# Optimization experiments

Measured on AMD Instinct MI355X. Metric: run time of the kernel, lower is better.

Reference implementation:

```python
import jax, jax.numpy as jnp
import numpy as np

B, N1, N2, C, P, H, MLP = 8, 4096, 4096, 512, 256, 8, 2048
HD = C // H  # head dim = 64
EPS = 1e-12


def _l2norm(x):
    # torch F.normalize(dim=-1): x / max(||x||_2, eps)
    n = jnp.sqrt(jnp.sum(x * x, axis=-1, keepdims=True))
    return x / jnp.maximum(n, EPS)


def setup_inputs() -> dict:
    key = jax.random.key(0)
    ks = jax.random.split(key, 8)
    w = lambda i, shape: jax.random.normal(ks[i], shape, jnp.float32) * 0.02
    return {
        "x1": jax.random.normal(ks[0], (B, N1, C), jnp.float32),
        "x2": jax.random.normal(ks[1], (B, N2, C), jnp.float32),
        "Wq": w(2, (C, C)), "bq": jnp.zeros((C,), jnp.float32),
        "Wkv": w(3, (C, 2 * C)), "bkv": jnp.zeros((2 * C,), jnp.float32),
        # proj_k and proj_v share ONE Linear(N_2, proj_size) in the source
        "Wp": w(4, (N2, P)), "bp": jnp.zeros((P,), jnp.float32),
        "pos_q": jnp.zeros((1, N1, C), jnp.float32),
        "pos_k": jnp.zeros((1, N2, C), jnp.float32),
        "temperature": jnp.ones((H, 1, 1), jnp.float32),
        "W1": w(5, (C, MLP)), "b1": jnp.zeros((MLP,), jnp.float32),
        "W2": w(6, (MLP, C)), "b2": jnp.zeros((C,), jnp.float32),
    }


def reference(x1, x2, Wq, bq, Wkv, bkv, Wp, bp, pos_q, pos_k, temperature,
              W1, b1, W2, b2):
    # q += pos_embed_q is in-place in torch, so q_skip includes pos embedding
    q = x1 @ Wq + bq + pos_q                      # [B,N1,C]
    q_skip = q
    kv = x2 @ Wkv + bkv                           # [B,N2,2C]
    k = kv[..., :C] + pos_k                       # [B,N2,C]
    v = kv[..., C:]                               # [B,N2,C]

    qh = q.reshape(B, N1, H, HD).transpose(0, 2, 1, 3)   # [B,H,N1,hd]
    kh = k.reshape(B, N2, H, HD).transpose(0, 2, 1, 3)   # [B,H,N2,hd]
    vh = v.reshape(B, N2, H, HD).transpose(0, 2, 1, 3)   # [B,H,N2,hd]

    # project K^T and V^T along the sequence axis (shared weights)
    kp = jnp.einsum('bhnd,np->bhdp', kh, Wp) + bp        # [B,H,hd,P]
    vp_t = jnp.einsum('bhnd,np->bhdp', vh, Wp) + bp      # [B,H,hd,P]

    attn = jnp.einsum('bhqd,bhdp->bhqp', qh, kp) * temperature  # [B,H,N1,P]
    attn = jax.nn.softmax(attn, axis=-1)                 # dropout: eval mode

    x = jnp.einsum('bhqp,bhdp->bhqd', attn, vp_t)        # [B,H,N1,hd]
    # source does permute(0,3,1,2).reshape(B,N1,C) -- replicate exactly
    x = x.transpose(0, 3, 1, 2).reshape(B, N1, C)

    x = _l2norm(x + q_skip)                              # Add & L2-Norm
    h = jax.nn.gelu(x @ W1 + b1, approximate=False)      # nn.GELU (exact)
    out = _l2norm(h @ W2 + b2 + x)                       # FFN -> Add & L2-Norm
    return out
```

## Files before the change

kernel.cpp:

```cpp
#include <hip/hip_runtime.h>
#include <hip/hip_bf16.h>
#include <math.h>

#define B_    8
#define N1_   4096
#define N2_   4096
#define C_    512
#define P_    256
#define H_    8
#define MLP_  2048
#define HD_   64

typedef __hip_bfloat16 bf16;
typedef __attribute__((ext_vector_type(8))) short short8;
typedef __attribute__((ext_vector_type(4))) float f32x4;

__device__ __forceinline__ float bf2f(bf16 v) { return __bfloat162float(v); }
__device__ __forceinline__ bf16  f2bf(float v) { return __float2bfloat16(v); }
__device__ __forceinline__ float ubf2f(unsigned short u) {
  union { float f; unsigned int i; } cv; cv.i = ((unsigned int)u) << 16; return cv.f;
}
__device__ __forceinline__ unsigned short f2bfu(float v) {
  union { bf16 b; unsigned short u; } cv; cv.b = __float2bfloat16(v); return cv.u;
}
__device__ __forceinline__ float gelu_fast(float x) {
  const float u = fabsf(x) * 0.70710678118654752f;
  const float t = __builtin_amdgcn_rcpf(__builtin_fmaf(0.3275911f, u, 1.0f));
  float p = __builtin_fmaf(1.061405429f, t, -1.453152027f);
  p = __builtin_fmaf(p, t, 1.421413741f);
  p = __builtin_fmaf(p, t, -0.284496736f);
  p = __builtin_fmaf(p, t, 0.254829592f);
  p *= t;
  const float e = __expf(-u * u);
  float erfv = __builtin_fmaf(-p, e, 1.0f);
  erfv = (x < 0.0f) ? -erfv : erfv;
  return 0.5f * x * (1.0f + erfv);
}

__device__ __forceinline__ void gload16(const void* g, void* l) {
  __builtin_amdgcn_global_load_lds(
      (const __attribute__((address_space(1))) void*)g,
      (__attribute__((address_space(3))) void*)l, 16, 0, 0);
}

__global__ __launch_bounds__(256) void f2b_kernel(
    const float* __restrict__ in, bf16* __restrict__ out, int n4)
{
  int i = blockIdx.x * 256 + threadIdx.x;
  const int stride = gridDim.x * 256;
  for (; i < n4; i += stride) {
    const float4 v = ((const float4*)in)[i];
    ushort4 o;
    o.x = f2bfu(v.x); o.y = f2bfu(v.y); o.z = f2bfu(v.z); o.w = f2bfu(v.w);
    ((ushort4*)out)[i] = o;
  }
}

__global__ __launch_bounds__(256) void transpose_f2b_kernel(
    const float* __restrict__ in, bf16* __restrict__ out, int K, int N, int ldin)
{
  __shared__ float tile[32][33];
  const int kb = blockIdx.y * 32, nb = blockIdx.x * 32;
  const int tx = threadIdx.x & 31, ty = threadIdx.x >> 5;
  #pragma unroll
  for (int i = 0; i < 4; ++i)
    tile[ty + 8 * i][tx] = in[(size_t)(kb + ty + 8 * i) * ldin + nb + tx];
  __syncthreads();
  #pragma unroll
  for (int i = 0; i < 4; ++i)
    out[(size_t)(nb + ty + 8 * i) * K + kb + tx] = f2bf(tile[tx][ty + 8 * i]);
}

template<int BN, int OUTF32, int ACT, int POS, int TRANSC>
__global__ __launch_bounds__(256) void mfma_gemm_kernel(
    const bf16* __restrict__ A, const bf16* __restrict__ Bt,
    const float* __restrict__ bias, const float* __restrict__ pos, int posmask,
    void* __restrict__ Cv, int M, int N, int K)
{
  constexpr int WGN = BN / 64;
  constexpr int WGR = 4 / WGN;
  constexpr int FM  = 128 / (16 * WGR);
  __shared__ bf16 As[128 * 32];
  __shared__ bf16 Bs[BN * 32];
  const int t  = threadIdx.x;
  const int l  = t & 63;
  const int w  = t >> 6;
  const int wr = w / WGN, wc = w % WGN;
  const int lr = l & 15, kg = l >> 4;

  const int gx  = gridDim.x;
  const int nwg = gx * gridDim.y;
  const int h   = blockIdx.y * gx + blockIdx.x;
  int bx = blockIdx.x, by = blockIdx.y;
  if ((nwg & 7) == 0) {
    const int tid = (h & 7) * (nwg >> 3) + (h >> 3);
    bx = tid % gx; by = tid / gx;
  }
  const int m0 = by * 128, n0 = bx * BN;

  const bf16* ga = A  + (size_t)(m0 + (t >> 2)) * K + (t & 3) * 8;
  const bf16* gb = Bt + (size_t)(n0 + (t >> 2)) * K + (t & 3) * 8;
  char* asl = (char*)As + t * 16;
  char* bsl = (char*)Bs + t * 16;

  f32x4 acc[FM][4] = {};

  for (int k0 = 0; k0 < K; k0 += 32) {
    gload16(ga, asl);
    gload16(ga + (size_t)64 * K, asl + 4096);
    gload16(gb, bsl);
    if (BN == 128) gload16(gb + (size_t)64 * K, bsl + 4096);
    ga += 32; gb += 32;
    __syncthreads();
    short8 af[FM], bfv[4];
    #pragma unroll
    for (int i = 0; i < FM; ++i)
      af[i] = *(const short8*)&As[(wr * (FM * 16) + i * 16 + lr) * 32 + kg * 8];
    #pragma unroll
    for (int j = 0; j < 4; ++j)
      bfv[j] = *(const short8*)&Bs[(wc * 64 + j * 16 + lr) * 32 + kg * 8];
    #pragma unroll
    for (int i = 0; i < FM; ++i)
      #pragma unroll
      for (int j = 0; j < 4; ++j)
        acc[i][j] = __builtin_amdgcn_mfma_f32_16x16x32_bf16(
            af[i], bfv[j], acc[i][j], 0, 0, 0);
    __syncthreads();
  }

  #pragma unroll
  for (int i = 0; i < FM; ++i) {
    #pragma unroll
    for (int j = 0; j < 4; ++j) {
      const int n = n0 + wc * 64 + j * 16 + lr;
      const float bv = bias[n];
      if (TRANSC) {
        const int mb = m0 + wr * (FM * 16) + i * 16 + kg * 4;
        ushort4 pk;
        #pragma unroll
        for (int r = 0; r < 4; ++r) {
          const int m = mb + r;
          float v = acc[i][j][r] + bv;
          if (POS) v += pos[(size_t)(m & posmask) * N + n];
          ((unsigned short*)&pk)[r] = f2bfu(v);
        }
        *(ushort4*)&((bf16*)Cv)[((size_t)(mb >> 12) * N + n) * (size_t)N1_ + (mb & 4095)] = pk;
      } else {
        #pragma unroll
        for (int r = 0; r < 4; ++r) {
          const int m = m0 + wr * (FM * 16) + i * 16 + kg * 4 + r;
          float v = acc[i][j][r] + bv;
          if (POS) v += pos[(size_t)(m & posmask) * N + n];
          if (ACT) v = gelu_fast(v);
          if (OUTF32) ((float*)Cv)[(size_t)m * N + n] = v;
          else        ((bf16*)Cv)[(size_t)m * N + n] = f2bf(v);
        }
      }
    }
  }
}

template<int BIASM>
__global__ __launch_bounds__(256) void proj_kernel(
    const bf16* __restrict__ A, const bf16* __restrict__ Bt,
    const float* __restrict__ bias, bf16* __restrict__ Cb,
    int M, int N, int K, long aBatch, long bBatch, long cBatch)
{
  __shared__ bf16 As[64 * 32];
  __shared__ bf16 Bs[64 * 32];
  const int t = threadIdx.x, l = t & 63, w = t >> 6;
  const int wr = w >> 1, wc = w & 1;
  const int lr = l & 15, kg = l >> 4;
  const int z = blockIdx.z;
  const int m0 = blockIdx.y * 64, n0 = blockIdx.x * 64;
  const bf16* ga = A  + (size_t)z * aBatch + (size_t)(m0 + (t >> 2)) * K + (t & 3) * 8;
  const bf16* gb = Bt + (size_t)z * bBatch + (size_t)(n0 + (t >> 2)) * K + (t & 3) * 8;
  char* asl = (char*)As + t * 16;
  char* bsl = (char*)Bs + t * 16;
  f32x4 acc[2][2] = {};
  for (int k0 = 0; k0 < K; k0 += 32) {
    gload16(ga, asl);
    gload16(gb, bsl);
    ga += 32; gb += 32;
    __syncthreads();
    short8 af[2], bfr[2];
    #pragma unroll
    for (int i = 0; i < 2; ++i)
      af[i] = *(const short8*)&As[(wr * 32 + i * 16 + lr) * 32 + kg * 8];
    #pragma unroll
    for (int j = 0; j < 2; ++j)
      bfr[j] = *(const short8*)&Bs[(wc * 32 + j * 16 + lr) * 32 + kg * 8];
    #pragma unroll
    for (int i = 0; i < 2; ++i)
      #pragma unroll
      for (int j = 0; j < 2; ++j)
        acc[i][j] = __builtin_amdgcn_mfma_f32_16x16x32_bf16(
            af[i], bfr[j], acc[i][j], 0, 0, 0);
    __syncthreads();
  }
  #pragma unroll
  for (int i = 0; i < 2; ++i)
    #pragma unroll
    for (int j = 0; j < 2; ++j) {
      const int n = n0 + wc * 32 + j * 16 + lr;
      #pragma unroll
      for (int r = 0; r < 4; ++r) {
        const int m = m0 + wr * 32 + i * 16 + kg * 4 + r;
        const float v = acc[i][j][r] + (BIASM ? bias[m] : bias[n]);
        Cb[(size_t)z * cBatch + (size_t)m * N + n] = f2bf(v);
      }
    }
}

__global__ __launch_bounds__(256) void attn_mfma_kernel(
    const bf16* __restrict__ qb, const bf16* __restrict__ kpT,
    const bf16* __restrict__ vp, const float* __restrict__ temp,
    bf16* __restrict__ xatT)
{
  __shared__ bf16 qs[64 * 64];
  __shared__ bf16 us[256 * 64];
  __shared__ bf16 vs[64 * 256];
  const int t = threadIdx.x, w = t >> 6, l = t & 63;
  const int lr = l & 15, kg = l >> 4;
  const int b = blockIdx.z, h = blockIdx.y;
  const int q0 = blockIdx.x * 64;
  const int bh = b * H_ + h;
  const float tv = temp[h];

  {
    const int rowb = t >> 3, ch = t & 7;
    #pragma unroll
    for (int p = 0; p < 2; ++p) {
      const int r = rowb + 32 * p;
      const short8 v = *(const short8*)(qb + ((size_t)(b * N1_ + q0 + r)) * C_ + h * HD_ + ch * 8);
      *(short8*)((char*)qs + ((r * 128 + ch * 16) ^ ((r & 7) << 4))) = v;
    }
    const bf16* kpb = kpT + (size_t)bh * (P_ * HD_);
    #pragma unroll
    for (int p = 0; p < 8; ++p) {
      const int r = rowb + 32 * p;
      const short8 v = *(const short8*)(kpb + r * HD_ + ch * 8);
      *(short8*)((char*)us + ((r * 128 + ch * 16) ^ ((r & 7) << 4))) = v;
    }
    const bf16* vpb = vp + (size_t)bh * (HD_ * P_);
    const int rowv = t >> 5, chv = t & 31;
    #pragma unroll
    for (int p = 0; p < 8; ++p) {
      const int r = rowv + 8 * p;
      const short8 v = *(const short8*)(vpb + r * P_ + chv * 8);
      *(short8*)((char*)vs + ((r * 512 + chv * 16) ^ ((r & 7) << 4))) = v;
    }
  }
  __syncthreads();

  short8 aq[2];
  {
    const int row = w * 16 + lr;
    const int sw = (row & 7) << 4;
    aq[0] = *(const short8*)((const char*)qs + ((row * 128 +  0 + kg * 16) ^ sw));
    aq[1] = *(const short8*)((const char*)qs + ((row * 128 + 64 + kg * 16) ^ sw));
  }
  f32x4 s[16] = {};
  #pragma unroll
  for (int j = 0; j < 16; ++j) {
    const int row = j * 16 + lr;
    const int sw = (row & 7) << 4;
    const short8 b0 = *(const short8*)((const char*)us + ((row * 128 +  0 + kg * 16) ^ sw));
    const short8 b1 = *(const short8*)((const char*)us + ((row * 128 + 64 + kg * 16) ^ sw));
    s[j] = __builtin_amdgcn_mfma_f32_16x16x32_bf16(aq[0], b0, s[j], 0, 0, 0);
    s[j] = __builtin_amdgcn_mfma_f32_16x16x32_bf16(aq[1], b1, s[j], 0, 0, 0);
  }

  float inv_[4];
  #pragma unroll
  for (int j = 0; j < 16; ++j)
    #pragma unroll
    for (int r = 0; r < 4; ++r) s[j][r] *= tv;
  #pragma unroll
  for (int r = 0; r < 4; ++r) {
    float m = s[0][r];
    #pragma unroll
    for (int j = 1; j < 16; ++j) m = fmaxf(m, s[j][r]);
    #pragma unroll
    for (int off = 1; off < 16; off <<= 1) m = fmaxf(m, __shfl_xor(m, off));
    float sum = 0.f;
    #pragma unroll
    for (int j = 0; j < 16; ++j) { s[j][r] = __expf(s[j][r] - m); sum += s[j][r]; }
    #pragma unroll
    for (int off = 1; off < 16; off <<= 1) sum += __shfl_xor(sum, off);
    inv_[r] = 1.0f / sum;
  }
  __syncthreads();

  #pragma unroll
  for (int r = 0; r < 4; ++r) {
    const int q = w * 16 + kg * 4 + r;
    const int sw = (q & 7) << 4;
    #pragma unroll
    for (int j = 0; j < 16; ++j) {
      const int p = j * 16 + lr;
      ((unsigned short*)us)[((q * 512 + p * 2) ^ sw) >> 1] = f2bfu(s[j][r] * inv_[r]);
    }
  }
  __syncthreads();

  f32x4 o[4] = {};
  #pragma unroll
  for (int kc = 0; kc < 8; ++kc) {
    const int qrow = w * 16 + lr;
    const short8 pb = *(const short8*)((const char*)us +
        ((qrow * 512 + kc * 64 + kg * 16) ^ ((qrow & 7) << 4)));
    #pragma unroll
    for (int i = 0; i < 4; ++i) {
      const int drow = i * 16 + lr;
      const short8 vb = *(const short8*)((const char*)vs +
          ((drow * 512 + kc * 64 + kg * 16) ^ ((drow & 7) << 4)));
      o[i] = __builtin_amdgcn_mfma_f32_16x16x32_bf16(vb, pb, o[i], 0, 0, 0);
    }
  }
  const int qq = q0 + w * 16 + lr;
  bf16* ob = xatT + (size_t)bh * (HD_ * (size_t)N1_) + qq;
  #pragma unroll
  for (int i = 0; i < 4; ++i)
    #pragma unroll
    for (int r = 0; r < 4; ++r) {
      const int d = i * 16 + kg * 4 + r;
      ob[(size_t)d * N1_] = f2bf(o[i][r]);
    }
}

__global__ __launch_bounds__(256) void norm1_kernel(
    const bf16* __restrict__ xatT, const bf16* __restrict__ qb,
    bf16* __restrict__ xb)
{
  const int row = blockIdx.x;
  const int b = row >> 12, np = row & 4095;
  const int d = np >> 6, h = (np >> 3) & 7, qhi = np & 7;
  const int c = threadIdx.x * 2;
  const size_t tbase = ((size_t)(b * H_ + h) * HD_ + d) * N1_ + qhi * 512 + c;
  const size_t qbase = (size_t)row * C_ + c;
  const ushort2 xa = *(const ushort2*)((const unsigned short*)xatT + tbase);
  const ushort2 qa = *(const ushort2*)((const unsigned short*)qb + qbase);
  float v0 = ubf2f(xa.x) + ubf2f(qa.x);
  float v1 = ubf2f(xa.y) + ubf2f(qa.y);
  float ss = v0 * v0 + v1 * v1;
  #pragma unroll
  for (int off = 32; off > 0; off >>= 1) ss += __shfl_xor(ss, off);
  __shared__ float sw[4];
  if ((threadIdx.x & 63) == 0) sw[threadIdx.x >> 6] = ss;
  __syncthreads();
  const float tot = sw[0] + sw[1] + sw[2] + sw[3];
  const float scale = 1.0f / fmaxf(sqrtf(tot), 1e-12f);
  ushort2 o;
  o.x = f2bfu(v0 * scale);
  o.y = f2bfu(v1 * scale);
  *(ushort2*)((unsigned short*)xb + qbase) = o;
}

__global__ __launch_bounds__(256) void norm2_kernel(
    const float* __restrict__ yb, const bf16* __restrict__ xb,
    float* __restrict__ outp)
{
  const int row = blockIdx.x;
  const int c0 = threadIdx.x, c1 = threadIdx.x + 256;
  float v0 = yb[(size_t)row * C_ + c0] + bf2f(xb[(size_t)row * C_ + c0]);
  float v1 = yb[(size_t)row * C_ + c1] + bf2f(xb[(size_t)row * C_ + c1]);
  float ss = v0 * v0 + v1 * v1;
  #pragma unroll
  for (int off = 32; off > 0; off >>= 1) ss += __shfl_xor(ss, off);
  __shared__ float sw[4];
  if ((threadIdx.x & 63) == 0) sw[threadIdx.x >> 6] = ss;
  __syncthreads();
  const float tot = sw[0] + sw[1] + sw[2] + sw[3];
  const float scale = 1.0f / fmaxf(sqrtf(tot), 1e-12f);
  outp[(size_t)row * C_ + c0] = v0 * scale;
  outp[(size_t)row * C_ + c1] = v1 * scale;
}

extern "C" void kernel_launch(void* const* d_in, const int* in_sizes, int n_in,
                              void* d_out, int out_size, void* d_ws, size_t ws_size,
                              hipStream_t stream)
{
  const float* x1   = (const float*)d_in[0];
  const float* x2   = (const float*)d_in[1];
  const float* Wq   = (const float*)d_in[2];
  const float* bq   = (const float*)d_in[3];
  const float* Wkv  = (const float*)d_in[4];
  const float* bkv  = (const float*)d_in[5];
  const float* Wp   = (const float*)d_in[6];
  const float* bp   = (const float*)d_in[7];
  const float* posq = (const float*)d_in[8];
  const float* posk = (const float*)d_in[9];
  const float* temp = (const float*)d_in[10];
  const float* W1   = (const float*)d_in[11];
  const float* b1   = (const float*)d_in[12];
  const float* W2   = (const float*)d_in[13];
  const float* b2   = (const float*)d_in[14];

  char* ws = (char*)d_ws;
  bf16*  Abuf = (bf16*)(ws);
  bf16*  Bbuf = (bf16*)(ws + 33554432);
  bf16*  Cbuf = (bf16*)(ws + 67108864);
  bf16*  kpT  = (bf16*)(ws + 100663296);
  bf16*  vpb  = (bf16*)(ws + 102760448);
  bf16*  WpT  = (bf16*)(ws + 104857600);
  bf16*  Wqt  = (bf16*)(ws + 106954752);
  bf16*  Wkt  = (bf16*)(ws + 107479040);
  bf16*  Wvt  = (bf16*)(ws + 108003328);
  float* outp = (float*)d_out;

  int CH;
  size_t w1t_off, w2t_off, yb_off;
  if (ws_size >= 239075328UL) {
    CH = 32768; w1t_off = 167772160UL; w2t_off = 169869312UL; yb_off = 171966464UL;
  } else if (ws_size >= 138412032UL) {
    CH = 16384; w1t_off = 100663296UL; w2t_off = 102760448UL; yb_off = 104857600UL;
  } else {
    CH = 8192;  w1t_off = 100663296UL; w2t_off = 102760448UL; yb_off = 106954752UL;
  }
  bf16*  W1t = (bf16*)(ws + w1t_off);
  bf16*  W2t = (bf16*)(ws + w2t_off);
  float* yb  = (float*)(ws + yb_off);

  const dim3 blk(256);
  const int Mrows = B_ * N1_;
  bf16* xatT = Bbuf;
  bf16* xb   = Abuf;
  bf16* hb   = Bbuf;
  bf16* qb   = Cbuf;

  f2b_kernel<<<dim3(2048), blk, 0, stream>>>(x2, Abuf, (B_ * N2_ * C_) / 4);
  transpose_f2b_kernel<<<dim3(16, 16), blk, 0, stream>>>(Wkv,      Wkt, C_, C_, 2 * C_);
  transpose_f2b_kernel<<<dim3(16, 16), blk, 0, stream>>>(Wkv + C_, Wvt, C_, C_, 2 * C_);
  transpose_f2b_kernel<<<dim3(16, 16), blk, 0, stream>>>(Wq,       Wqt, C_, C_, C_);
  transpose_f2b_kernel<<<dim3(8, 128), blk, 0, stream>>>(Wp,       WpT, N2_, P_, P_);

  mfma_gemm_kernel<128,0,0,1,1><<<dim3(C_/128, Mrows/128), blk, 0, stream>>>(
      Abuf, Wkt, bkv, posk, N2_ - 1, Cbuf, Mrows, C_, C_);
  proj_kernel<1><<<dim3(1, 4, B_*H_), blk, 0, stream>>>(
      WpT, Cbuf, bp, kpT, P_, HD_, N2_, 0L, (long)HD_*N2_, (long)P_*HD_);
  mfma_gemm_kernel<128,0,0,0,1><<<dim3(C_/128, Mrows/128), blk, 0, stream>>>(
      Abuf, Wvt, bkv + C_, nullptr, 0, Cbuf, Mrows, C_, C_);
  proj_kernel<0><<<dim3(4, 1, B_*H_), blk, 0, stream>>>(
      Cbuf, WpT, bp, vpb, HD_, P_, N2_, (long)HD_*N2_, 0L, (long)HD_*P_);
  f2b_kernel<<<dim3(2048), blk, 0, stream>>>(x1, Abuf, (B_ * N1_ * C_) / 4);
  mfma_gemm_kernel<128,0,0,1,0><<<dim3(C_/128, Mrows/128), blk, 0, stream>>>(
      Abuf, Wqt, bq, posq, N1_ - 1, qb, Mrows, C_, C_);
  attn_mfma_kernel<<<dim3(N1_/64, H_, B_), blk, 0, stream>>>(
      qb, kpT, vpb, temp, xatT);
  transpose_f2b_kernel<<<dim3(64, 16), blk, 0, stream>>>(W1, W1t, C_,   MLP_, MLP_);
  transpose_f2b_kernel<<<dim3(16, 64), blk, 0, stream>>>(W2, W2t, MLP_, C_,   C_);
  norm1_kernel<<<dim3(Mrows), blk, 0, stream>>>(xatT, qb, xb);
  for (int c = 0; c < Mrows / CH; ++c) {
    const bf16* xc = xb + (size_t)c * CH * C_;
    mfma_gemm_kernel<128,0,1,0,0><<<dim3(MLP_/128, CH/128), blk, 0, stream>>>(
        xc, W1t, b1, nullptr, 0, hb, CH, MLP_, C_);
    mfma_gemm_kernel<128,1,0,0,0><<<dim3(C_/128, CH/128), blk, 0, stream>>>(
        hb, W2t, b2, nullptr, 0, yb, CH, C_, MLP_);
    norm2_kernel<<<dim3(CH), blk, 0, stream>>>(
        yb, xc, outp + (size_t)c * CH * C_);
  }
}
```

Baseline: 773.4 us.

## Double-buffer LDS in GEMM and projection kernels; fuse K/V GEMMs

Both the main MFMA GEMM and the projection kernel now use two LDS buffers. The next K-slice is loaded while the current one is computed, hiding global-load latency behind the MFMAs. The separate K and V input GEMMs are merged into one GEMM over the concatenated Wkv, with the transposed output split into two buffers (K into Cbuf, V into Bbuf). This removes one kernel launch and one re-read of x2, at the cost of doubled LDS per block, which may lower occupancy.

```diff
diff --git a/kernel.cpp b/kernel.cpp
--- a/kernel.cpp
+++ b/kernel.cpp
@@ -75,13 +75,13 @@
 __global__ __launch_bounds__(256) void mfma_gemm_kernel(
     const bf16* __restrict__ A, const bf16* __restrict__ Bt,
     const float* __restrict__ bias, const float* __restrict__ pos, int posmask,
-    void* __restrict__ Cv, int M, int N, int K)
+    void* __restrict__ Cv, void* __restrict__ Cv2, int M, int N, int K)
 {
   constexpr int WGN = BN / 64;
   constexpr int WGR = 4 / WGN;
   constexpr int FM  = 128 / (16 * WGR);
-  __shared__ bf16 As[128 * 32];
-  __shared__ bf16 Bs[BN * 32];
+  __shared__ bf16 As[2][128 * 32];
+  __shared__ bf16 Bs[2][BN * 32];
   const int t  = threadIdx.x;
   const int l  = t & 63;
   const int w  = t >> 6;
@@ -100,33 +100,48 @@
 
   const bf16* ga = A  + (size_t)(m0 + (t >> 2)) * K + (t & 3) * 8;
   const bf16* gb = Bt + (size_t)(n0 + (t >> 2)) * K + (t & 3) * 8;
-  char* asl = (char*)As + t * 16;
-  char* bsl = (char*)Bs + t * 16;
+  char* asl0 = (char*)As[0] + t * 16;
+  char* asl1 = (char*)As[1] + t * 16;
+  char* bsl0 = (char*)Bs[0] + t * 16;
+  char* bsl1 = (char*)Bs[1] + t * 16;
 
   f32x4 acc[FM][4] = {};
 
-  for (int k0 = 0; k0 < K; k0 += 32) {
-    gload16(ga, asl);
-    gload16(ga + (size_t)64 * K, asl + 4096);
-    gload16(gb, bsl);
-    if (BN == 128) gload16(gb + (size_t)64 * K, bsl + 4096);
-    ga += 32; gb += 32;
+#define STAGEK(bufi, koff) do {                                         \
+    gload16(ga + (koff), asl##bufi);                                    \
+    gload16(ga + (koff) + (size_t)64 * K, asl##bufi + 4096);            \
+    gload16(gb + (koff), bsl##bufi);                                    \
+    if (BN == 128) gload16(gb + (koff) + (size_t)64 * K, bsl##bufi + 4096); \
+  } while (0)
+
+#define COMPUTEK(bufi) do {                                             \
+    short8 af[FM], bfv[4];                                              \
+    _Pragma("unroll")                                                   \
+    for (int i = 0; i < FM; ++i)                                        \
+      af[i] = *(const short8*)&As[bufi][(wr*(FM*16)+i*16+lr)*32 + kg*8];\
+    _Pragma("unroll")                                                   \
+    for (int j = 0; j < 4; ++j)                                         \
+      bfv[j] = *(const short8*)&Bs[bufi][(wc*64+j*16+lr)*32 + kg*8];    \
+    _Pragma("unroll")                                                   \
+    for (int i = 0; i < FM; ++i)                                        \
+      _Pragma("unroll")                                                 \
+      for (int j = 0; j < 4; ++j)                                       \
+        acc[i][j] = __builtin_amdgcn_mfma_f32_16x16x32_bf16(            \
+            af[i], bfv[j], acc[i][j], 0, 0, 0);                         \
+  } while (0)
+
+  STAGEK(0, 0);
+  __syncthreads();
+  for (int k0 = 0; k0 < K; k0 += 64) {
+    STAGEK(1, k0 + 32);
+    COMPUTEK(0);
     __syncthreads();
-    short8 af[FM], bfv[4];
-    #pragma unroll
-    for (int i = 0; i < FM; ++i)
-      af[i] = *(const short8*)&As[(wr * (FM * 16) + i * 16 + lr) * 32 + kg * 8];
-    #pragma unroll
-    for (int j = 0; j < 4; ++j)
-      bfv[j] = *(const short8*)&Bs[(wc * 64 + j * 16 + lr) * 32 + kg * 8];
-    #pragma unroll
-    for (int i = 0; i < FM; ++i)
-      #pragma unroll
-      for (int j = 0; j < 4; ++j)
-        acc[i][j] = __builtin_amdgcn_mfma_f32_16x16x32_bf16(
-            af[i], bfv[j], acc[i][j], 0, 0, 0);
+    if (k0 + 64 < K) STAGEK(0, k0 + 64);
+    COMPUTEK(1);
     __syncthreads();
   }
+#undef STAGEK
+#undef COMPUTEK
 
   #pragma unroll
   for (int i = 0; i < FM; ++i) {
@@ -139,12 +154,13 @@
         ushort4 pk;
         #pragma unroll
         for (int r = 0; r < 4; ++r) {
-          const int m = mb + r;
           float v = acc[i][j][r] + bv;
-          if (POS) v += pos[(size_t)(m & posmask) * N + n];
+          if (POS && n < C_) v += pos[(size_t)((mb + r) & posmask) * C_ + n];
           ((unsigned short*)&pk)[r] = f2bfu(v);
         }
-        *(ushort4*)&((bf16*)Cv)[((size_t)(mb >> 12) * N + n) * (size_t)N1_ + (mb & 4095)] = pk;
+        bf16* ob = (bf16*)(n < C_ ? Cv : Cv2);
+        const int nc = n & (C_ - 1);
+        *(ushort4*)&ob[((size_t)(mb >> 12) * C_ + nc) * (size_t)N1_ + (mb & 4095)] = pk;
       } else {
         #pragma unroll
         for (int r = 0; r < 4; ++r) {
@@ -166,8 +182,8 @@
     const float* __restrict__ bias, bf16* __restrict__ Cb,
     int M, int N, int K, long aBatch, long bBatch, long cBatch)
 {
-  __shared__ bf16 As[64 * 32];
-  __shared__ bf16 Bs[64 * 32];
+  __shared__ bf16 As[2][64 * 32];
+  __shared__ bf16 Bs[2][64 * 32];
   const int t = threadIdx.x, l = t & 63, w = t >> 6;
   const int wr = w >> 1, wc = w & 1;
   const int lr = l & 15, kg = l >> 4;
@@ -175,29 +191,46 @@
   const int m0 = blockIdx.y * 64, n0 = blockIdx.x * 64;
   const bf16* ga = A  + (size_t)z * aBatch + (size_t)(m0 + (t >> 2)) * K + (t & 3) * 8;
   const bf16* gb = Bt + (size_t)z * bBatch + (size_t)(n0 + (t >> 2)) * K + (t & 3) * 8;
-  char* asl = (char*)As + t * 16;
-  char* bsl = (char*)Bs + t * 16;
+  char* asl0 = (char*)As[0] + t * 16;
+  char* asl1 = (char*)As[1] + t * 16;
+  char* bsl0 = (char*)Bs[0] + t * 16;
+  char* bsl1 = (char*)Bs[1] + t * 16;
   f32x4 acc[2][2] = {};
-  for (int k0 = 0; k0 < K; k0 += 32) {
-    gload16(ga, asl);
-    gload16(gb, bsl);
-    ga += 32; gb += 32;
+
+#define PSTAGE(bufi, koff) do {                  \
+    gload16(ga + (koff), asl##bufi);             \
+    gload16(gb + (koff), bsl##bufi);             \
+  } while (0)
+
+#define PCOMP(bufi) do {                                                \
+    short8 af[2], bfr[2];                                               \
+    _Pragma("unroll")                                                   \
+    for (int i = 0; i < 2; ++i)                                         \
+      af[i] = *(const short8*)&As[bufi][(wr*32+i*16+lr)*32 + kg*8];     \
+    _Pragma("unroll")                                                   \
+    for (int j = 0; j < 2; ++j)                                         \
+      bfr[j] = *(const short8*)&Bs[bufi][(wc*32+j*16+lr)*32 + kg*8];    \
+    _Pragma("unroll")                                                   \
+    for (int i = 0; i < 2; ++i)                                         \
+      _Pragma("unroll")                                                 \
+      for (int j = 0; j < 2; ++j)                                       \
+        acc[i][j] = __builtin_amdgcn_mfma_f32_16x16x32_bf16(            \
+            af[i], bfr[j], acc[i][j], 0, 0, 0);                         \
+  } while (0)
+
+  PSTAGE(0, 0);
+  __syncthreads();
+  for (int k0 = 0; k0 < K; k0 += 64) {
+    PSTAGE(1, k0 + 32);
+    PCOMP(0);
     __syncthreads();
-    short8 af[2], bfr[2];
-    #pragma unroll
-    for (int i = 0; i < 2; ++i)
-      af[i] = *(const short8*)&As[(wr * 32 + i * 16 + lr) * 32 + kg * 8];
-    #pragma unroll
-    for (int j = 0; j < 2; ++j)
-      bfr[j] = *(const short8*)&Bs[(wc * 32 + j * 16 + lr) * 32 + kg * 8];
-    #pragma unroll
-    for (int i = 0; i < 2; ++i)
-      #pragma unroll
-      for (int j = 0; j < 2; ++j)
-        acc[i][j] = __builtin_amdgcn_mfma_f32_16x16x32_bf16(
-            af[i], bfr[j], acc[i][j], 0, 0, 0);
+    if (k0 + 64 < K) PSTAGE(0, k0 + 64);
+    PCOMP(1);
     __syncthreads();
   }
+#undef PSTAGE
+#undef PCOMP
+
   #pragma unroll
   for (int i = 0; i < 2; ++i)
     #pragma unroll
@@ -405,8 +438,7 @@
   bf16*  vpb  = (bf16*)(ws + 102760448);
   bf16*  WpT  = (bf16*)(ws + 104857600);
   bf16*  Wqt  = (bf16*)(ws + 106954752);
-  bf16*  Wkt  = (bf16*)(ws + 107479040);
-  bf16*  Wvt  = (bf16*)(ws + 108003328);
+  bf16*  Wkvt = (bf16*)(ws + 107479040);
   float* outp = (float*)d_out;
 
   int CH;
@@ -428,24 +460,23 @@
   bf16* xb   = Abuf;
   bf16* hb   = Bbuf;
   bf16* qb   = Cbuf;
+  bf16* kT   = Cbuf;
+  bf16* vT   = Bbuf;
 
   f2b_kernel<<<dim3(2048), blk, 0, stream>>>(x2, Abuf, (B_ * N2_ * C_) / 4);
-  transpose_f2b_kernel<<<dim3(16, 16), blk, 0, stream>>>(Wkv,      Wkt, C_, C_, 2 * C_);
-  transpose_f2b_kernel<<<dim3(16, 16), blk, 0, stream>>>(Wkv + C_, Wvt, C_, C_, 2 * C_);
-  transpose_f2b_kernel<<<dim3(16, 16), blk, 0, stream>>>(Wq,       Wqt, C_, C_, C_);
-  transpose_f2b_kernel<<<dim3(8, 128), blk, 0, stream>>>(Wp,       WpT, N2_, P_, P_);
-
-  mfma_gemm_kernel<128,0,0,1,1><<<dim3(C_/128, Mrows/128), blk, 0, stream>>>(
-      Abuf, Wkt, bkv, posk, N2_ - 1, Cbuf, Mrows, C_, C_);
+  transpose_f2b_kernel<<<dim3(32, 16), blk, 0, stream>>>(Wkv, Wkvt, C_, 2 * C_, 2 * C_);
+  transpose_f2b_kernel<<<dim3(16, 16), blk, 0, stream>>>(Wq,  Wqt,  C_, C_,     C_);
+  transpose_f2b_kernel<<<dim3(8, 128), blk, 0, stream>>>(Wp,  WpT,  N2_, P_,    P_);
+
+  mfma_gemm_kernel<128,0,0,1,1><<<dim3((2*C_)/128, Mrows/128), blk, 0, stream>>>(
+      Abuf, Wkvt, bkv, posk, N2_ - 1, kT, vT, Mrows, 2 * C_, C_);
   proj_kernel<1><<<dim3(1, 4, B_*H_), blk, 0, stream>>>(
-      WpT, Cbuf, bp, kpT, P_, HD_, N2_, 0L, (long)HD_*N2_, (long)P_*HD_);
-  mfma_gemm_kernel<128,0,0,0,1><<<dim3(C_/128, Mrows/128), blk, 0, stream>>>(
-      Abuf, Wvt, bkv + C_, nullptr, 0, Cbuf, Mrows, C_, C_);
+      WpT, kT, bp, kpT, P_, HD_, N2_, 0L, (long)HD_*N2_, (long)P_*HD_);
   proj_kernel<0><<<dim3(4, 1, B_*H_), blk, 0, stream>>>(
-      Cbuf, WpT, bp, vpb, HD_, P_, N2_, (long)HD_*N2_, 0L, (long)HD_*P_);
+      vT, WpT, bp, vpb, HD_, P_, N2_, (long)HD_*N2_, 0L, (long)HD_*P_);
   f2b_kernel<<<dim3(2048), blk, 0, stream>>>(x1, Abuf, (B_ * N1_ * C_) / 4);
   mfma_gemm_kernel<128,0,0,1,0><<<dim3(C_/128, Mrows/128), blk, 0, stream>>>(
-      Abuf, Wqt, bq, posq, N1_ - 1, qb, Mrows, C_, C_);
+      Abuf, Wqt, bq, posq, N1_ - 1, qb, nullptr, Mrows, C_, C_);
   attn_mfma_kernel<<<dim3(N1_/64, H_, B_), blk, 0, stream>>>(
       qb, kpT, vpb, temp, xatT);
   transpose_f2b_kernel<<<dim3(64, 16), blk, 0, stream>>>(W1, W1t, C_,   MLP_, MLP_);
@@ -454,9 +485,9 @@
   for (int c = 0; c < Mrows / CH; ++c) {
     const bf16* xc = xb + (size_t)c * CH * C_;
     mfma_gemm_kernel<128,0,1,0,0><<<dim3(MLP_/128, CH/128), blk, 0, stream>>>(
-        xc, W1t, b1, nullptr, 0, hb, CH, MLP_, C_);
+        xc, W1t, b1, nullptr, 0, hb, nullptr, CH, MLP_, C_);
     mfma_gemm_kernel<128,1,0,0,0><<<dim3(C_/128, CH/128), blk, 0, stream>>>(
-        hb, W2t, b2, nullptr, 0, yb, CH, C_, MLP_);
+        hb, W2t, b2, nullptr, 0, yb, nullptr, CH, C_, MLP_);
     norm2_kernel<<<dim3(CH), blk, 0, stream>>>(
         yb, xc, outp + (size_t)c * CH * C_);
   }
```

Result: no change. 780.3 us (+0.9%).
